# Performance work log

Hardware: AMD Instinct MI355X
Metric: run time of the kernel (lower is better)

Reference implementation:

```python
import jax, jax.numpy as jnp
import numpy as np

N = 100000
E = 1200000
F_IN = 64
H = 64
C = 10


def _gcn_norm(edge_idx):
    # PyG gcn_norm with add_self_loops=True, edge_weight=1
    src = jnp.concatenate([edge_idx[0], jnp.arange(N, dtype=edge_idx.dtype)])
    dst = jnp.concatenate([edge_idx[1], jnp.arange(N, dtype=edge_idx.dtype)])
    deg = jax.ops.segment_sum(jnp.ones_like(dst, dtype=jnp.float32), dst, num_segments=N)
    dinv = jnp.where(deg > 0, jax.lax.rsqrt(deg), 0.0)
    norm = dinv[src] * dinv[dst]  # [E+N]
    return src, dst, norm


def _gcn_conv(x, src, dst, norm, W, b):
    h = x @ W                               # [N, out]
    msg = h[src] * norm[:, None]            # gather + scale, [E+N, out]
    out = jax.ops.segment_sum(msg, dst, num_segments=N)  # scatter-add
    return out + b


def setup_inputs() -> dict:
    key = jax.random.key(0)
    ks = jax.random.split(key, 8)
    x = jax.random.normal(ks[0], (N, F_IN), dtype=jnp.float32)
    edge_idx = jax.random.randint(ks[1], (2, E), 0, N, dtype=jnp.int64 if jax.config.jax_enable_x64 else jnp.int32)
    def glorot(k, fan_in, fan_out):
        s = jnp.sqrt(6.0 / (fan_in + fan_out)).astype(jnp.float32)
        return jax.random.uniform(k, (fan_in, fan_out), jnp.float32, -s, s)
    W0 = glorot(ks[2], F_IN, H); b0 = jnp.zeros((H,), jnp.float32)
    W1 = glorot(ks[3], H, H);    b1 = jnp.zeros((H,), jnp.float32)
    W2 = glorot(ks[4], H, H);    b2 = jnp.zeros((H,), jnp.float32)
    Wl = glorot(ks[5], H, C);    bl = jnp.zeros((C,), jnp.float32)
    return {"x": x, "edge_idx": edge_idx, "W0": W0, "b0": b0,
            "W1": W1, "b1": b1, "W2": W2, "b2": b2, "Wl": Wl, "bl": bl}


def reference(x, edge_idx, W0, b0, W1, b1, W2, b2, Wl, bl):
    src, dst, norm = _gcn_norm(edge_idx)
    # conv0 + relu
    h = jax.nn.relu(_gcn_conv(x, src, dst, norm, W0, b0))
    # convs[0] + relu (i=0 < num_layers-2=1)
    h = jax.nn.relu(_gcn_conv(h, src, dst, norm, W1, b1))
    # convs[1], no relu (last)
    h = _gcn_conv(h, src, dst, norm, W2, b2)
    # global_add_pool(batch=None): sum over all nodes, keepdim -> [1, H]
    g = jnp.sum(h, axis=0, keepdims=True)
    # dropout is identity in eval mode
    return g @ Wl + bl  # [1, C]
```

## Files before the change

kernel.cpp:

```cpp
#include <hip/hip_runtime.h>
#include <hip/hip_bf16.h>

#define NN 100000
#define NE 1200000
#define NE4 (NE / 4)
#define XCD_N 8
#define NPX (NN / XCD_N)
#define CAP 32
#define SPILL_MAX 4096

typedef float floatx2 __attribute__((ext_vector_type(2)));

__global__ __launch_bounds__(256) void bucket_fill_kernel(const int* __restrict__ esrc,
                                                          const int* __restrict__ edst,
                                                          int* __restrict__ deg,
                                                          int* __restrict__ bucket,
                                                          int* __restrict__ spill,
                                                          int* __restrict__ spill_cnt) {
    int xcd = blockIdx.x & 7;
    int sub = blockIdx.x >> 3;
    int nsub = gridDim.x >> 3;
    int lo = xcd * NPX;
    for (int i = sub * 256 + threadIdx.x; i < NE4; i += nsub * 256) {
        int4 d  = ((const int4*)edst)[i];
        int4 sr = ((const int4*)esrc)[i];
        #pragma unroll
        for (int c = 0; c < 4; ++c) {
            int dd = (c == 0) ? d.x : (c == 1) ? d.y : (c == 2) ? d.z : d.w;
            int ss = (c == 0) ? sr.x : (c == 1) ? sr.y : (c == 2) ? sr.z : sr.w;
            if ((unsigned)(dd - lo) < NPX) {
                int slot = atomicAdd(&deg[dd], 1);
                if (slot < CAP) {
                    bucket[dd * CAP + slot] = ss;
                } else {
                    int p = atomicAdd(spill_cnt, 1);
                    if (p < SPILL_MAX) { spill[2 * p] = dd; spill[2 * p + 1] = ss; }
                }
            }
        }
    }
}

__device__ __forceinline__ unsigned char enc_fp8(float f) {
    int w = __builtin_amdgcn_cvt_pk_fp8_f32(f, f, 0, false);
    return (unsigned char)(w & 0xFF);
}

__device__ __forceinline__ void acc_fp8(float acc[8], uint2 v) {
    floatx2 a0 = __builtin_amdgcn_cvt_pk_f32_fp8((int)v.x, false);
    floatx2 a1 = __builtin_amdgcn_cvt_pk_f32_fp8((int)v.x, true);
    floatx2 a2 = __builtin_amdgcn_cvt_pk_f32_fp8((int)v.y, false);
    floatx2 a3 = __builtin_amdgcn_cvt_pk_f32_fp8((int)v.y, true);
    acc[0] += a0.x; acc[1] += a0.y;
    acc[2] += a1.x; acc[3] += a1.y;
    acc[4] += a2.x; acc[5] += a2.y;
    acc[6] += a3.x; acc[7] += a3.y;
}

__device__ __forceinline__ unsigned packbf2(float lof, float hif) {
    __hip_bfloat16 l = __float2bfloat16(lof), h = __float2bfloat16(hif);
    unsigned short ul, uh;
    __builtin_memcpy(&ul, &l, 2);
    __builtin_memcpy(&uh, &h, 2);
    return ((unsigned)uh << 16) | ul;
}

template <int MODE>
__global__ __launch_bounds__(256) void mm_kernel(const void* __restrict__ in,
                                                 const float* __restrict__ W,
                                                 const float* __restrict__ bias,
                                                 const int* __restrict__ deg,
                                                 unsigned char* __restrict__ uout) {
    __shared__ float Ws[64 * 64];
    __shared__ float hrow[4][64];
    int tid = threadIdx.x;
    {
        const float4* Wv = (const float4*)W;
        float4* Wsv = (float4*)Ws;
        #pragma unroll
        for (int i = 0; i < 4; ++i) Wsv[tid + 256 * i] = Wv[tid + 256 * i];
    }
    int local = tid >> 6;
    int f = tid & 63;
    int n = blockIdx.x * 4 + local;
    float din = rsqrtf((float)(deg[n] + 1));
    float v;
    if (MODE == 0) {
        v = ((const float*)in)[n * 64 + f];
    } else {
        v = __bfloat162float(((const __hip_bfloat16*)in)[n * 64 + f]);
        v = fmaxf(fmaf(din, v, bias[f]), 0.f);
    }
    hrow[local][f] = v;
    __syncthreads();
    float acc = 0.f;
    #pragma unroll
    for (int k = 0; k < 64; ++k)
        acc = fmaf(hrow[local][k], Ws[k * 64 + f], acc);
    uout[n * 64 + f] = enc_fp8(din * acc);
}

__device__ __forceinline__ void agg_row(const int* __restrict__ degv,
                                        const int* __restrict__ bucket,
                                        const uint2* __restrict__ u2,
                                        const int* __restrict__ spill,
                                        const int* __restrict__ spill_cnt,
                                        int n, int lane, int grp, int fo,
                                        float acc[8]) {
    float a1[8], a2[8], a3[8];
    #pragma unroll
    for (int i = 0; i < 8; ++i) { acc[i] = 0.f; a1[i] = 0.f; a2[i] = 0.f; a3[i] = 0.f; }
    int deg = degv[n];
    int dc = deg < CAP ? deg : CAP;
    int cidx = 0;
    if ((lane & 31) < dc) cidx = bucket[n * CAP + (lane & 31)];
    if (grp == 0) acc_fp8(acc, u2[n * 8 + fo]);
    int s0 = __shfl(cidx, grp);
    int s1 = __shfl(cidx, grp + 8);
    int s2 = __shfl(cidx, grp + 16);
    int s3 = __shfl(cidx, grp + 24);
    if (grp < dc)      acc_fp8(acc, u2[s0 * 8 + fo]);
    if (grp + 8 < dc)  acc_fp8(a1, u2[s1 * 8 + fo]);
    if (grp + 16 < dc) acc_fp8(a2, u2[s2 * 8 + fo]);
    if (grp + 24 < dc) acc_fp8(a3, u2[s3 * 8 + fo]);
    if (deg > CAP) {
        int cnt = *spill_cnt; if (cnt > SPILL_MAX) cnt = SPILL_MAX;
        for (int e = 0; e < cnt; ++e) {
            if (spill[2 * e] == n && grp == 0)
                acc_fp8(a3, u2[spill[2 * e + 1] * 8 + fo]);
        }
    }
    #pragma unroll
    for (int i = 0; i < 8; ++i) {
        float v = (acc[i] + a1[i]) + (a2[i] + a3[i]);
        v += __shfl_xor(v, 8);
        v += __shfl_xor(v, 16);
        v += __shfl_xor(v, 32);
        acc[i] = v;
    }
}

template <int POOL>
__global__ __launch_bounds__(256, 8) void agg_kernel(const int* __restrict__ degv,
                                                     const int* __restrict__ bucket,
                                                     const uint2* __restrict__ uin,
                                                     const int* __restrict__ spill,
                                                     const int* __restrict__ spill_cnt,
                                                     __hip_bfloat16* __restrict__ S,
                                                     float* __restrict__ gp) {
    __shared__ float gpart[64];
    int tid = threadIdx.x;
    if (POOL) {
        if (tid < 64) gpart[tid] = 0.f;
        __syncthreads();
    }
    int lane = tid & 63;
    int grp = lane >> 3;
    int fo = lane & 7;
    int n = blockIdx.x * 4 + (tid >> 6);
    float acc[8];
    agg_row(degv, bucket, uin, spill, spill_cnt, n, lane, grp, fo, acc);
    if (POOL) {
        if (grp == 0) {
            float din = rsqrtf((float)(degv[n] + 1));
            #pragma unroll
            for (int i = 0; i < 8; ++i) atomicAdd(&gpart[fo * 8 + i], din * acc[i]);
        }
        __syncthreads();
        if (tid < 64) atomicAdd(&gp[(blockIdx.x & 63) * 64 + tid], gpart[tid]);
    } else {
        if (grp == 0) {
            uint4 pv;
            pv.x = packbf2(acc[0], acc[1]);
            pv.y = packbf2(acc[2], acc[3]);
            pv.z = packbf2(acc[4], acc[5]);
            pv.w = packbf2(acc[6], acc[7]);
            ((uint4*)S)[n * 8 + fo] = pv;
        }
    }
}

__global__ __launch_bounds__(64) void head_kernel(const float* __restrict__ gp,
                                                  const float* __restrict__ b2,
                                                  const float* __restrict__ Wl,
                                                  const float* __restrict__ bl,
                                                  float* __restrict__ out) {
    int t = threadIdx.x;
    float s = 0.f;
    #pragma unroll 8
    for (int r = 0; r < 64; ++r) s += gp[r * 64 + t];
    float gf = s + (float)NN * b2[t];
    #pragma unroll
    for (int c = 0; c < 10; ++c) {
        float p = gf * Wl[t * 10 + c];
        #pragma unroll
        for (int off = 32; off > 0; off >>= 1) p += __shfl_down(p, off);
        if (t == 0) out[c] = p + bl[c];
    }
}

extern "C" void kernel_launch(void* const* d_in, const int* in_sizes, int n_in,
                              void* d_out, int out_size, void* d_ws, size_t ws_size,
                              hipStream_t stream) {
    const float* x  = (const float*)d_in[0];
    const int* eidx = (const int*)d_in[1];
    const int* esrc = eidx;
    const int* edst = eidx + NE;
    const float* W0 = (const float*)d_in[2];
    const float* b0 = (const float*)d_in[3];
    const float* W1 = (const float*)d_in[4];
    const float* b1 = (const float*)d_in[5];
    const float* W2 = (const float*)d_in[6];
    const float* b2 = (const float*)d_in[7];
    const float* Wl = (const float*)d_in[8];
    const float* bl = (const float*)d_in[9];
    float* out = (float*)d_out;

    float* ws = (float*)d_ws;
    size_t off = 0;
    int*   deg    = (int*)(ws + off); off += NN;
    unsigned char* ua = (unsigned char*)(ws + off); off += (size_t)NN * 16;
    unsigned char* ub = (unsigned char*)(ws + off); off += (size_t)NN * 16;
    __hip_bfloat16* S = (__hip_bfloat16*)(ws + off); off += (size_t)NN * 32;
    float* gp     =        ws + off;  off += 64 * 64;
    int*   spill_cnt = (int*)(ws + off); off += 4;
    int*   spill  = (int*)(ws + off); off += 2 * SPILL_MAX;
    int*   bucket = (int*)(ws + off); off += (size_t)NN * CAP;

    hipMemsetAsync(deg, 0, NN * sizeof(int), stream);
    hipMemsetAsync(gp, 0, (64 * 64 + 4) * sizeof(float), stream);

    bucket_fill_kernel<<<2048, 256, 0, stream>>>(esrc, edst, deg, bucket, spill, spill_cnt);

    mm_kernel<0><<<NN / 4, 256, 0, stream>>>(x, W0, nullptr, deg, ua);
    agg_kernel<0><<<NN / 4, 256, 0, stream>>>(deg, bucket, (const uint2*)ua, spill, spill_cnt, S, gp);
    mm_kernel<1><<<NN / 4, 256, 0, stream>>>(S, W1, b0, deg, ub);
    agg_kernel<0><<<NN / 4, 256, 0, stream>>>(deg, bucket, (const uint2*)ub, spill, spill_cnt, S, gp);
    mm_kernel<1><<<NN / 4, 256, 0, stream>>>(S, W2, b1, deg, ua);
    agg_kernel<1><<<NN / 4, 256, 0, stream>>>(deg, bucket, (const uint2*)ua, spill, spill_cnt, S, gp);
    head_kernel<<<1, 64, 0, stream>>>(gp, b2, Wl, bl, out);
}
```

Baseline: 343.5 us.

## Drop XCD-partitioned bucket fill and use packed float2 accumulation in aggregation

The bucket build no longer has each XCD group scan all edges and keep only destinations in its node range. Each thread now processes its share of edges once, with bucket writes done through atomicExch. This cuts the redundant reads of the edge list but gives up XCD-local atomics and L2 locality on deg and bucket. Aggregation also switches to floatx2 accumulators so the adds can map to packed FP32 instructions.

Result: slower. 398.6 us (+16.0%).

```diff
diff --git a/kernel.cpp b/kernel.cpp
--- a/kernel.cpp
+++ b/kernel.cpp
@@ -4,38 +4,30 @@
 #define NN 100000
 #define NE 1200000
 #define NE4 (NE / 4)
-#define XCD_N 8
-#define NPX (NN / XCD_N)
 #define CAP 32
 #define SPILL_MAX 4096
 
 typedef float floatx2 __attribute__((ext_vector_type(2)));
 
-__global__ __launch_bounds__(256) void bucket_fill_kernel(const int* __restrict__ esrc,
-                                                          const int* __restrict__ edst,
-                                                          int* __restrict__ deg,
-                                                          int* __restrict__ bucket,
-                                                          int* __restrict__ spill,
-                                                          int* __restrict__ spill_cnt) {
-    int xcd = blockIdx.x & 7;
-    int sub = blockIdx.x >> 3;
-    int nsub = gridDim.x >> 3;
-    int lo = xcd * NPX;
-    for (int i = sub * 256 + threadIdx.x; i < NE4; i += nsub * 256) {
+__global__ __launch_bounds__(256) void build_kernel(const int* __restrict__ esrc,
+                                                    const int* __restrict__ edst,
+                                                    int* __restrict__ deg,
+                                                    int* __restrict__ bucket,
+                                                    int* __restrict__ spill,
+                                                    int* __restrict__ spill_cnt) {
+    for (int i = blockIdx.x * 256 + threadIdx.x; i < NE4; i += gridDim.x * 256) {
         int4 d  = ((const int4*)edst)[i];
         int4 sr = ((const int4*)esrc)[i];
         #pragma unroll
         for (int c = 0; c < 4; ++c) {
             int dd = (c == 0) ? d.x : (c == 1) ? d.y : (c == 2) ? d.z : d.w;
             int ss = (c == 0) ? sr.x : (c == 1) ? sr.y : (c == 2) ? sr.z : sr.w;
-            if ((unsigned)(dd - lo) < NPX) {
-                int slot = atomicAdd(&deg[dd], 1);
-                if (slot < CAP) {
-                    bucket[dd * CAP + slot] = ss;
-                } else {
-                    int p = atomicAdd(spill_cnt, 1);
-                    if (p < SPILL_MAX) { spill[2 * p] = dd; spill[2 * p + 1] = ss; }
-                }
+            int slot = atomicAdd(&deg[dd], 1);
+            if (slot < CAP) {
+                atomicExch(&bucket[dd * CAP + slot], ss);
+            } else {
+                int p = atomicAdd(spill_cnt, 1);
+                if (p < SPILL_MAX) { spill[2 * p] = dd; spill[2 * p + 1] = ss; }
             }
         }
     }
@@ -46,15 +38,11 @@
     return (unsigned char)(w & 0xFF);
 }
 
-__device__ __forceinline__ void acc_fp8(float acc[8], uint2 v) {
-    floatx2 a0 = __builtin_amdgcn_cvt_pk_f32_fp8((int)v.x, false);
-    floatx2 a1 = __builtin_amdgcn_cvt_pk_f32_fp8((int)v.x, true);
-    floatx2 a2 = __builtin_amdgcn_cvt_pk_f32_fp8((int)v.y, false);
-    floatx2 a3 = __builtin_amdgcn_cvt_pk_f32_fp8((int)v.y, true);
-    acc[0] += a0.x; acc[1] += a0.y;
-    acc[2] += a1.x; acc[3] += a1.y;
-    acc[4] += a2.x; acc[5] += a2.y;
-    acc[6] += a3.x; acc[7] += a3.y;
+__device__ __forceinline__ void acc_fp8v(floatx2 acc[4], uint2 v) {
+    acc[0] += __builtin_amdgcn_cvt_pk_f32_fp8((int)v.x, false);
+    acc[1] += __builtin_amdgcn_cvt_pk_f32_fp8((int)v.x, true);
+    acc[2] += __builtin_amdgcn_cvt_pk_f32_fp8((int)v.y, false);
+    acc[3] += __builtin_amdgcn_cvt_pk_f32_fp8((int)v.y, true);
 }
 
 __device__ __forceinline__ unsigned packbf2(float lof, float hif) {
@@ -106,37 +94,45 @@
                                         const int* __restrict__ spill,
                                         const int* __restrict__ spill_cnt,
                                         int n, int lane, int grp, int fo,
-                                        float acc[8]) {
-    float a1[8], a2[8], a3[8];
-    #pragma unroll
-    for (int i = 0; i < 8; ++i) { acc[i] = 0.f; a1[i] = 0.f; a2[i] = 0.f; a3[i] = 0.f; }
+                                        floatx2 acc[4]) {
+    floatx2 a1[4], a2[4], a3[4];
+    #pragma unroll
+    for (int i = 0; i < 4; ++i) {
+        acc[i] = (floatx2)(0.f); a1[i] = (floatx2)(0.f);
+        a2[i] = (floatx2)(0.f);  a3[i] = (floatx2)(0.f);
+    }
     int deg = degv[n];
     int dc = deg < CAP ? deg : CAP;
     int cidx = 0;
     if ((lane & 31) < dc) cidx = bucket[n * CAP + (lane & 31)];
-    if (grp == 0) acc_fp8(acc, u2[n * 8 + fo]);
+    if (grp == 0) acc_fp8v(acc, u2[n * 8 + fo]);
     int s0 = __shfl(cidx, grp);
     int s1 = __shfl(cidx, grp + 8);
     int s2 = __shfl(cidx, grp + 16);
     int s3 = __shfl(cidx, grp + 24);
-    if (grp < dc)      acc_fp8(acc, u2[s0 * 8 + fo]);
-    if (grp + 8 < dc)  acc_fp8(a1, u2[s1 * 8 + fo]);
-    if (grp + 16 < dc) acc_fp8(a2, u2[s2 * 8 + fo]);
-    if (grp + 24 < dc) acc_fp8(a3, u2[s3 * 8 + fo]);
+    if (grp < dc)      acc_fp8v(acc, u2[s0 * 8 + fo]);
+    if (grp + 8 < dc)  acc_fp8v(a1, u2[s1 * 8 + fo]);
+    if (grp + 16 < dc) acc_fp8v(a2, u2[s2 * 8 + fo]);
+    if (grp + 24 < dc) acc_fp8v(a3, u2[s3 * 8 + fo]);
     if (deg > CAP) {
         int cnt = *spill_cnt; if (cnt > SPILL_MAX) cnt = SPILL_MAX;
         for (int e = 0; e < cnt; ++e) {
             if (spill[2 * e] == n && grp == 0)
-                acc_fp8(a3, u2[spill[2 * e + 1] * 8 + fo]);
-        }
-    }
-    #pragma unroll
-    for (int i = 0; i < 8; ++i) {
-        float v = (acc[i] + a1[i]) + (a2[i] + a3[i]);
-        v += __shfl_xor(v, 8);
-        v += __shfl_xor(v, 16);
-        v += __shfl_xor(v, 32);
-        acc[i] = v;
+                acc_fp8v(a3, u2[spill[2 * e + 1] * 8 + fo]);
+        }
+    }
+    #pragma unroll
+    for (int i = 0; i < 4; ++i)
+        acc[i] = (acc[i] + a1[i]) + (a2[i] + a3[i]);
+    #pragma unroll
+    for (int L = 8; L <= 32; L <<= 1) {
+        #pragma unroll
+        for (int i = 0; i < 4; ++i) {
+            floatx2 t;
+            t.x = __shfl_xor(acc[i].x, L);
+            t.y = __shfl_xor(acc[i].y, L);
+            acc[i] += t;
+        }
     }
 }
 
@@ -158,23 +154,26 @@
     int grp = lane >> 3;
     int fo = lane & 7;
     int n = blockIdx.x * 4 + (tid >> 6);
-    float acc[8];
+    floatx2 acc[4];
     agg_row(degv, bucket, uin, spill, spill_cnt, n, lane, grp, fo, acc);
     if (POOL) {
         if (grp == 0) {
             float din = rsqrtf((float)(degv[n] + 1));
             #pragma unroll
-            for (int i = 0; i < 8; ++i) atomicAdd(&gpart[fo * 8 + i], din * acc[i]);
+            for (int i = 0; i < 4; ++i) {
+                atomicAdd(&gpart[fo * 8 + 2 * i],     din * acc[i].x);
+                atomicAdd(&gpart[fo * 8 + 2 * i + 1], din * acc[i].y);
+            }
         }
         __syncthreads();
         if (tid < 64) atomicAdd(&gp[(blockIdx.x & 63) * 64 + tid], gpart[tid]);
     } else {
         if (grp == 0) {
             uint4 pv;
-            pv.x = packbf2(acc[0], acc[1]);
-            pv.y = packbf2(acc[2], acc[3]);
-            pv.z = packbf2(acc[4], acc[5]);
-            pv.w = packbf2(acc[6], acc[7]);
+            pv.x = packbf2(acc[0].x, acc[0].y);
+            pv.y = packbf2(acc[1].x, acc[1].y);
+            pv.z = packbf2(acc[2].x, acc[2].y);
+            pv.w = packbf2(acc[3].x, acc[3].y);
             ((uint4*)S)[n * 8 + fo] = pv;
         }
     }
@@ -230,7 +229,7 @@
     hipMemsetAsync(deg, 0, NN * sizeof(int), stream);
     hipMemsetAsync(gp, 0, (64 * 64 + 4) * sizeof(float), stream);
 
-    bucket_fill_kernel<<<2048, 256, 0, stream>>>(esrc, edst, deg, bucket, spill, spill_cnt);
+    build_kernel<<<2048, 256, 0, stream>>>(esrc, edst, deg, bucket, spill, spill_cnt);
 
     mm_kernel<0><<<NN / 4, 256, 0, stream>>>(x, W0, nullptr, deg, ua);
     agg_kernel<0><<<NN / 4, 256, 0, stream>>>(deg, bucket, (const uint2*)ua, spill, spill_cnt, S, gp);
```
